# Performance work log

Measured on AMD Instinct MI355X. Metric: run time of the kernel, lower is better.

The kernel has to match this reference:

```python
import jax, jax.numpy as jnp
import numpy as np

EPS = 1e-5

def _instance_norm(x):
    # PyG InstanceNorm with batch=None, affine=False: per-channel normalize
    # over the node/edge dimension with biased variance.
    mean = jnp.mean(x, axis=0, keepdims=True)
    var = jnp.mean(jnp.square(x - mean), axis=0, keepdims=True)
    return (x - mean) * jax.lax.rsqrt(var + EPS)

def setup_inputs() -> dict:
    key = jax.random.key(0)
    ks = jax.random.split(key, 8)
    N, E, H = 50000, 800000, 64
    s1 = 1.0 / np.sqrt(2 * H)
    s2 = 1.0 / np.sqrt(4 * H)
    s3 = 1.0 / np.sqrt(H)
    return {
        "emb": jax.random.normal(ks[0], (N, H), dtype=jnp.float32),
        "edge_index": jax.random.randint(ks[1], (2, E), 0, N, dtype=jnp.int64),
        "W1": jax.random.normal(ks[2], (2 * H, 4 * H), dtype=jnp.float32) * s1,
        "b1": jnp.zeros((4 * H,), dtype=jnp.float32),
        "W2": jax.random.normal(ks[3], (4 * H, H), dtype=jnp.float32) * s2,
        "b2": jnp.zeros((H,), dtype=jnp.float32),
        "W3": jax.random.normal(ks[4], (H, 1), dtype=jnp.float32) * s3,
        "b3": jnp.zeros((1,), dtype=jnp.float32),
    }

def reference(emb, edge_index, W1, b1, W2, b2, W3, b3):
    # Dropout is identity in eval mode.
    col, row = edge_index[0], edge_index[1]
    f12 = jnp.concatenate([emb[col], emb[row]], axis=-1)  # [E, 2H]
    h = jax.nn.relu(_instance_norm(f12 @ W1 + b1))        # [E, 4H]
    h = jax.nn.relu(_instance_norm(h @ W2 + b2))          # [E, H]
    return h @ W3 + b3                                    # [E, 1]
```

## Files before the change

kernel.cpp:

```cpp
#include <hip/hip_runtime.h>
#include <stdint.h>

#define EPS 1e-5f

typedef __attribute__((ext_vector_type(8))) short bf16x8;
typedef __attribute__((ext_vector_type(4))) float f32x4;

__device__ __forceinline__ short f2bf(float f) {
  union { float f; unsigned u; } c; c.f = f;
  unsigned r = (c.u + 0x7FFFu + ((c.u >> 16) & 1u)) >> 16;
  return (short)r;
}
__device__ __forceinline__ float bf2f(unsigned short s) {
  union { unsigned u; float f; } c; c.u = ((unsigned)s) << 16;
  return c.f;
}

#define ASYNC_COPY16(gsrc, ldst)                                                   \
  __builtin_amdgcn_global_load_lds(                                                \
      (const __attribute__((address_space(1))) void*)(gsrc),                       \
      (__attribute__((address_space(3))) void*)(ldst), 16, 0, 0)

#define WS_SUM1 0
#define WS_SQ1  256
#define WS_SUM2 512
#define WS_SQ2  576
#define WS_M1   640
#define WS_I1   896
#define WS_M2   1152
#define WS_I2   1216
#define H2S_BYTE_OFF 8192

__global__ void k_zero(float* ws) {
  for (int i = threadIdx.x; i < 640; i += 256) ws[i] = 0.f;
}

__global__ void k_finalize(float* ws, int n, int so, int qo, int mo, int io, float invE) {
  int j = threadIdx.x;
  if (j < n) {
    float m = ws[so + j] * invE;
    float var = ws[qo + j] * invE - m * m;
    ws[mo + j] = m;
    ws[io + j] = rsqrtf(var + EPS);
  }
}

__global__ __launch_bounds__(256, 2) void k_pass_a(
    const float* __restrict__ emb, const int* __restrict__ ei,
    const float* __restrict__ W1, const float* __restrict__ b1,
    float* __restrict__ ws, char* __restrict__ h1img, int E) {
  extern __shared__ __align__(16) char lds[];
  const int tid = threadIdx.x;
  const int lane = tid & 63;
  const int w = tid >> 6;
  const int l15 = lane & 15;
  const int l4 = lane >> 4;

  bf16x8 B1[4][4];
#pragma unroll
  for (int ni = 0; ni < 4; ++ni)
#pragma unroll
    for (int kk = 0; kk < 4; ++kk) {
      const int c = w * 64 + ni * 16 + l15;
      const int kb = kk * 32 + l4 * 8;
      bf16x8 v;
#pragma unroll
      for (int i = 0; i < 8; ++i) v[i] = f2bf(W1[(kb + i) * 256 + c]);
      B1[ni][kk] = v;
    }
  float b1v[4];
#pragma unroll
  for (int ni = 0; ni < 4; ++ni) b1v[ni] = b1[w * 64 + ni * 16 + l15];

  float sAcc[4] = {0, 0, 0, 0}, qAcc[4] = {0, 0, 0, 0};

  const int nTiles = E >> 6;
  const int e_ = tid >> 2, q_ = tid & 3;

  float4 pf[8];
  {
    const int e0 = blockIdx.x << 6;
    const int nidx = (q_ < 2) ? ei[e0 + e_] : ei[E + e0 + e_];
    const float* src = emb + (long)nidx * 64 + (q_ & 1) * 32;
#pragma unroll
    for (int jj = 0; jj < 8; ++jj)
      pf[jj] = *reinterpret_cast<const float4*>(src + jj * 4);
  }

  for (int t = blockIdx.x; t < nTiles; t += gridDim.x) {
#pragma unroll
    for (int jj = 0; jj < 4; ++jj) {
      bf16x8 p;
      p[0] = f2bf(pf[2 * jj].x); p[1] = f2bf(pf[2 * jj].y);
      p[2] = f2bf(pf[2 * jj].z); p[3] = f2bf(pf[2 * jj].w);
      p[4] = f2bf(pf[2 * jj + 1].x); p[5] = f2bf(pf[2 * jj + 1].y);
      p[6] = f2bf(pf[2 * jj + 1].z); p[7] = f2bf(pf[2 * jj + 1].w);
      int byte = e_ * 256 + q_ * 64 + jj * 16;
      byte ^= (e_ & 7) << 4;
      *reinterpret_cast<bf16x8*>(lds + byte) = p;
    }
    __syncthreads();

    {
      const int tn = t + (int)gridDim.x;
      const int tv = (tn < nTiles) ? tn : t;
      const int e0n = tv << 6;
      const int nidx = (q_ < 2) ? ei[e0n + e_] : ei[E + e0n + e_];
      const float* src = emb + (long)nidx * 64 + (q_ & 1) * 32;
#pragma unroll
      for (int jj = 0; jj < 8; ++jj)
        pf[jj] = *reinterpret_cast<const float4*>(src + jj * 4);
    }

    f32x4 acc[4][4];
#pragma unroll
    for (int mi = 0; mi < 4; ++mi)
#pragma unroll
      for (int ni = 0; ni < 4; ++ni) acc[mi][ni] = f32x4{0.f, 0.f, 0.f, 0.f};
#pragma unroll
    for (int kk = 0; kk < 4; ++kk) {
      bf16x8 af[4];
#pragma unroll
      for (int mi = 0; mi < 4; ++mi) {
        const int row = mi * 16 + l15;
        int byte = row * 256 + kk * 64 + l4 * 16;
        byte ^= (row & 7) << 4;
        af[mi] = *reinterpret_cast<const bf16x8*>(lds + byte);
      }
#pragma unroll
      for (int ni = 0; ni < 4; ++ni)
#pragma unroll
        for (int mi = 0; mi < 4; ++mi)
          acc[mi][ni] = __builtin_amdgcn_mfma_f32_16x16x32_bf16(af[mi], B1[ni][kk], acc[mi][ni], 0, 0, 0);
    }

    char* g = lds + 16384;
#pragma unroll
    for (int mi = 0; mi < 4; ++mi)
#pragma unroll
      for (int ni = 0; ni < 4; ++ni) {
        const int c = w * 64 + ni * 16 + l15;
#pragma unroll
        for (int r = 0; r < 4; ++r) {
          const int row = mi * 16 + l4 * 4 + r;
          const short vb = f2bf(acc[mi][ni][r] + b1v[ni]);
          const float vr = bf2f((unsigned short)vb);
          sAcc[ni] += vr;
          qAcc[ni] += vr * vr;
          int byte = row * 512 + c * 2;
          byte ^= (row & 7) << 4;
          *reinterpret_cast<short*>(g + byte) = vb;
        }
      }
    __syncthreads();

    {
      const char* srcL = lds + 16384 + w * 8192;
      char* dstG = h1img + (size_t)t * 32768 + w * 8192;
#pragma unroll
      for (int r = 0; r < 8; ++r) {
        const bf16x8 v = *reinterpret_cast<const bf16x8*>(srcL + r * 1024 + lane * 16);
        __builtin_nontemporal_store(v, reinterpret_cast<bf16x8*>(dstG + r * 1024 + lane * 16));
      }
    }
  }

#pragma unroll
  for (int ni = 0; ni < 4; ++ni) {
    float s = sAcc[ni], q = qAcc[ni];
    s += __shfl_xor(s, 16); s += __shfl_xor(s, 32);
    q += __shfl_xor(q, 16); q += __shfl_xor(q, 32);
    if (lane < 16) {
      atomicAdd(&ws[WS_SUM1 + w * 64 + ni * 16 + lane], s);
      atomicAdd(&ws[WS_SQ1 + w * 64 + ni * 16 + lane], q);
    }
  }
}

__global__ __launch_bounds__(256, 4) void k_pass_b(
    const char* __restrict__ h1img, const float* __restrict__ W2,
    const float* __restrict__ b2, float* __restrict__ ws,
    unsigned short* __restrict__ h2s, int E) {
  extern __shared__ __align__(16) char lds[];
  const int tid = threadIdx.x;
  const int lane = tid & 63;
  const int w = tid >> 6;
  const int l15 = lane & 15;
  const int l4 = lane >> 4;

  bf16x8 B2[8];
#pragma unroll
  for (int kk = 0; kk < 8; ++kk) {
    const int c = w * 16 + l15;
    const int kb = kk * 32 + l4 * 8;
    bf16x8 v;
#pragma unroll
    for (int i = 0; i < 8; ++i) v[i] = f2bf(W2[(kb + i) * 64 + c]);
    B2[kk] = v;
  }
  const float b2v = b2[w * 16 + l15];

  reinterpret_cast<float*>(lds + 32768)[tid] = ws[WS_M1 + tid];
  reinterpret_cast<float*>(lds + 33792)[tid] = ws[WS_I1 + tid];

  float s2A = 0.f, q2A = 0.f;
  const int nTiles = E >> 6;

  for (int t = blockIdx.x; t < nTiles; t += gridDim.x) {
    __syncthreads();

    {
      const char* src = h1img + (size_t)t * 32768 + w * 8192 + lane * 16;
      char* dst = lds + w * 8192;
#pragma unroll
      for (int r = 0; r < 8; ++r)
        ASYNC_COPY16(src + r * 1024, dst + r * 1024);
    }
    __syncthreads();

    f32x4 acc2[4];
#pragma unroll
    for (int mi = 0; mi < 4; ++mi) acc2[mi] = f32x4{0.f, 0.f, 0.f, 0.f};
#pragma unroll
    for (int kk = 0; kk < 8; ++kk) {
      const int cb = (kk * 32 + l4 * 8) * 4;
      const float4 m1a = *reinterpret_cast<const float4*>(lds + 32768 + cb);
      const float4 m1b = *reinterpret_cast<const float4*>(lds + 32768 + cb + 16);
      const float4 i1a = *reinterpret_cast<const float4*>(lds + 33792 + cb);
      const float4 i1b = *reinterpret_cast<const float4*>(lds + 33792 + cb + 16);
      const float mv[8] = {m1a.x, m1a.y, m1a.z, m1a.w, m1b.x, m1b.y, m1b.z, m1b.w};
      const float iv[8] = {i1a.x, i1a.y, i1a.z, i1a.w, i1b.x, i1b.y, i1b.z, i1b.w};
#pragma unroll
      for (int mi = 0; mi < 4; ++mi) {
        const int row = mi * 16 + l15;
        int byte = row * 512 + kk * 64 + l4 * 16;
        byte ^= (row & 7) << 4;
        const bf16x8 a = *reinterpret_cast<const bf16x8*>(lds + byte);
        bf16x8 an;
#pragma unroll
        for (int i = 0; i < 8; ++i) {
          float v = bf2f((unsigned short)a[i]);
          v = (v - mv[i]) * iv[i];
          an[i] = f2bf(v > 0.f ? v : 0.f);
        }
        acc2[mi] = __builtin_amdgcn_mfma_f32_16x16x32_bf16(an, B2[kk], acc2[mi], 0, 0, 0);
      }
    }
    __syncthreads();

#pragma unroll
    for (int mi = 0; mi < 4; ++mi)
#pragma unroll
      for (int r = 0; r < 4; ++r) {
        const int row = mi * 16 + l4 * 4 + r;
        const float v = acc2[mi][r] + b2v;
        s2A += v;
        q2A += v * v;
        int byte = row * 128 + (w * 16 + l15) * 2;
        byte ^= ((row >> 2) & 3) << 5;
        *reinterpret_cast<short*>(lds + byte) = f2bf(v);
      }
    __syncthreads();

    {
      const int row = tid >> 2, ch = tid & 3;
      const int rb = row * 128 + ((ch * 32) ^ (((row >> 2) & 3) << 5));
      const bf16x8 v0 = *reinterpret_cast<const bf16x8*>(lds + rb);
      const bf16x8 v1 = *reinterpret_cast<const bf16x8*>(lds + rb + 16);
      char* dstG = (char*)h2s + (size_t)t * 8192 + row * 128 + ch * 32;
      __builtin_nontemporal_store(v0, reinterpret_cast<bf16x8*>(dstG));
      __builtin_nontemporal_store(v1, reinterpret_cast<bf16x8*>(dstG + 16));
    }
  }

  {
    float s = s2A, q = q2A;
    s += __shfl_xor(s, 16); s += __shfl_xor(s, 32);
    q += __shfl_xor(q, 16); q += __shfl_xor(q, 32);
    if (lane < 16) {
      atomicAdd(&ws[WS_SUM2 + w * 16 + lane], s);
      atomicAdd(&ws[WS_SQ2 + w * 16 + lane], q);
    }
  }
}

template <int MODE>
__global__ __launch_bounds__(256, 2) void fused_pass(
    const float* __restrict__ emb, const int* __restrict__ ei,
    const float* __restrict__ W1, const float* __restrict__ b1,
    const float* __restrict__ W2, const float* __restrict__ b2,
    const float* __restrict__ W3, const float* __restrict__ b3,
    float* __restrict__ ws, unsigned short* __restrict__ h2s,
    float* __restrict__ out, int E, int storeH2) {
  extern __shared__ __align__(16) char lds[];
  const int tid = threadIdx.x;
  const int lane = tid & 63;
  const int w = tid >> 6;
  const int l15 = lane & 15;
  const int l4 = lane >> 4;

  bf16x8 B1[4][4];
#pragma unroll
  for (int ni = 0; ni < 4; ++ni)
#pragma unroll
    for (int kk = 0; kk < 4; ++kk) {
      const int c = w * 64 + ni * 16 + l15;
      const int kb = kk * 32 + l4 * 8;
      bf16x8 v;
#pragma unroll
      for (int i = 0; i < 8; ++i) v[i] = f2bf(W1[(kb + i) * 256 + c]);
      B1[ni][kk] = v;
    }
  float b1v[4], m1v[4] = {0, 0, 0, 0}, i1v[4] = {0, 0, 0, 0};
#pragma unroll
  for (int ni = 0; ni < 4; ++ni) {
    const int c = w * 64 + ni * 16 + l15;
    b1v[ni] = b1[c];
    if (MODE >= 1) { m1v[ni] = ws[WS_M1 + c]; i1v[ni] = ws[WS_I1 + c]; }
  }
  bf16x8 B2[8];
  float b2v = 0.f, m2v = 0.f, i2v = 0.f, w3v = 0.f;
  if (MODE >= 1) {
#pragma unroll
    for (int kk = 0; kk < 8; ++kk) {
      const int c = w * 16 + l15;
      const int kb = kk * 32 + l4 * 8;
      bf16x8 v;
#pragma unroll
      for (int i = 0; i < 8; ++i) v[i] = f2bf(W2[(kb + i) * 64 + c]);
      B2[kk] = v;
    }
    b2v = b2[w * 16 + l15];
    if (MODE == 2) {
      m2v = ws[WS_M2 + w * 16 + l15];
      i2v = ws[WS_I2 + w * 16 + l15];
      w3v = W3[w * 16 + l15];
    }
  }

  float sAcc[4] = {0, 0, 0, 0}, qAcc[4] = {0, 0, 0, 0};
  float s2A = 0.f, q2A = 0.f;

  const int nTiles = E >> 6;
  for (int t = blockIdx.x; t < nTiles; t += gridDim.x) {
    const int e0 = t << 6;
    __syncthreads();

    {
      const int e = tid >> 2, q = tid & 3;
      const int nidx = (q < 2) ? ei[e0 + e] : ei[E + e0 + e];
      const float* src = emb + (long)nidx * 64 + (q & 1) * 32;
#pragma unroll
      for (int jj = 0; jj < 4; ++jj) {
        float4 fa = *reinterpret_cast<const float4*>(src + jj * 8);
        float4 fb = *reinterpret_cast<const float4*>(src + jj * 8 + 4);
        bf16x8 p;
        p[0] = f2bf(fa.x); p[1] = f2bf(fa.y); p[2] = f2bf(fa.z); p[3] = f2bf(fa.w);
        p[4] = f2bf(fb.x); p[5] = f2bf(fb.y); p[6] = f2bf(fb.z); p[7] = f2bf(fb.w);
        int byte = e * 256 + q * 64 + jj * 16;
        byte ^= (e & 7) << 4;
        *reinterpret_cast<bf16x8*>(lds + byte) = p;
      }
      if (MODE == 2) {
        if (tid < 64) reinterpret_cast<float*>(lds + 49152)[tid] = 0.f;
      }
    }
    __syncthreads();

    f32x4 acc[4][4];
#pragma unroll
    for (int mi = 0; mi < 4; ++mi)
#pragma unroll
      for (int ni = 0; ni < 4; ++ni) acc[mi][ni] = f32x4{0.f, 0.f, 0.f, 0.f};
#pragma unroll
    for (int kk = 0; kk < 4; ++kk) {
      bf16x8 af[4];
#pragma unroll
      for (int mi = 0; mi < 4; ++mi) {
        const int row = mi * 16 + l15;
        int byte = row * 256 + kk * 64 + l4 * 16;
        byte ^= (row & 7) << 4;
        af[mi] = *reinterpret_cast<const bf16x8*>(lds + byte);
      }
#pragma unroll
      for (int ni = 0; ni < 4; ++ni)
#pragma unroll
        for (int mi = 0; mi < 4; ++mi)
          acc[mi][ni] = __builtin_amdgcn_mfma_f32_16x16x32_bf16(af[mi], B1[ni][kk], acc[mi][ni], 0, 0, 0);
    }

    if (MODE == 0) {
#pragma unroll
      for (int mi = 0; mi < 4; ++mi)
#pragma unroll
        for (int ni = 0; ni < 4; ++ni)
#pragma unroll
          for (int r = 0; r < 4; ++r) {
            const float v = acc[mi][ni][r] + b1v[ni];
            sAcc[ni] += v;
            qAcc[ni] += v * v;
          }
    } else {
      char* g = lds + 16384;
#pragma unroll
      for (int mi = 0; mi < 4; ++mi)
#pragma unroll
        for (int ni = 0; ni < 4; ++ni) {
          const int c = w * 64 + ni * 16 + l15;
#pragma unroll
          for (int r = 0; r < 4; ++r) {
            const int row = mi * 16 + l4 * 4 + r;
            float v = (acc[mi][ni][r] + b1v[ni] - m1v[ni]) * i1v[ni];
            v = v > 0.f ? v : 0.f;
            int byte = row * 512 + c * 2;
            byte ^= (row & 7) << 4;
            *reinterpret_cast<short*>(g + byte) = f2bf(v);
          }
        }
      __syncthreads();

      f32x4 acc2[4];
#pragma unroll
      for (int mi = 0; mi < 4; ++mi) acc2[mi] = f32x4{0.f, 0.f, 0.f, 0.f};
#pragma unroll
      for (int kk = 0; kk < 8; ++kk) {
#pragma unroll
        for (int mi = 0; mi < 4; ++mi) {
          const int row = mi * 16 + l15;
          int byte = row * 512 + kk * 64 + l4 * 16;
          byte ^= (row & 7) << 4;
          const bf16x8 a2 = *reinterpret_cast<const bf16x8*>(g + byte);
          acc2[mi] = __builtin_amdgcn_mfma_f32_16x16x32_bf16(a2, B2[kk], acc2[mi], 0, 0, 0);
        }
      }

      if (MODE == 1) {
#pragma unroll
        for (int mi = 0; mi < 4; ++mi)
#pragma unroll
          for (int r = 0; r < 4; ++r) {
            const float v = acc2[mi][r] + b2v;
            s2A += v;
            q2A += v * v;
            if (storeH2) {
              const int row = e0 + mi * 16 + l4 * 4 + r;
              h2s[(size_t)row * 64 + w * 16 + l15] = (unsigned short)f2bf(v);
            }
          }
      } else {
        float* outp = reinterpret_cast<float*>(lds + 49152);
#pragma unroll
        for (int mi = 0; mi < 4; ++mi)
#pragma unroll
          for (int r = 0; r < 4; ++r) {
            const float v = acc2[mi][r] + b2v;
            float z = (v - m2v) * i2v;
            z = z > 0.f ? z : 0.f;
            float pv = z * w3v;
            pv += __shfl_xor(pv, 1);
            pv += __shfl_xor(pv, 2);
            pv += __shfl_xor(pv, 4);
            pv += __shfl_xor(pv, 8);
            if (l15 == 0) atomicAdd(&outp[mi * 16 + l4 * 4 + r], pv);
          }
        __syncthreads();
        if (tid < 64) out[e0 + tid] = outp[tid] + b3[0];
      }
    }
  }

  if (MODE == 0) {
#pragma unroll
    for (int ni = 0; ni < 4; ++ni) {
      float s = sAcc[ni], q = qAcc[ni];
      s += __shfl_xor(s, 16); s += __shfl_xor(s, 32);
      q += __shfl_xor(q, 16); q += __shfl_xor(q, 32);
      if (lane < 16) {
        atomicAdd(&ws[WS_SUM1 + w * 64 + ni * 16 + lane], s);
        atomicAdd(&ws[WS_SQ1 + w * 64 + ni * 16 + lane], q);
      }
    }
  }
  if (MODE == 1) {
    float s = s2A, q = q2A;
    s += __shfl_xor(s, 16); s += __shfl_xor(s, 32);
    q += __shfl_xor(q, 16); q += __shfl_xor(q, 32);
    if (lane < 16) {
      atomicAdd(&ws[WS_SUM2 + w * 16 + lane], s);
      atomicAdd(&ws[WS_SQ2 + w * 16 + lane], q);
    }
  }
}

__global__ void k_out(const unsigned short* __restrict__ h2s, const float* __restrict__ ws,
                      const float* __restrict__ W3, const float* __restrict__ b3,
                      float* __restrict__ out, int E) {
  __shared__ float sm[64], si[64], sw[64];
  const int tid = threadIdx.x;
  if (tid < 64) {
    sm[tid] = ws[WS_M2 + tid];
    si[tid] = ws[WS_I2 + tid];
    sw[tid] = W3[tid];
  }
  __syncthreads();
  const int e = blockIdx.x * 256 + tid;
  if (e >= E) return;
  const unsigned short* rp = h2s + (size_t)e * 64;
  float a = 0.f;
#pragma unroll
  for (int jj = 0; jj < 8; ++jj) {
    const bf16x8 v8 = *reinterpret_cast<const bf16x8*>(rp + jj * 8);
#pragma unroll
    for (int i = 0; i < 8; ++i) {
      const int j = jj * 8 + i;
      const float v = bf2f((unsigned short)v8[i]);
      float z = (v - sm[j]) * si[j];
      z = z > 0.f ? z : 0.f;
      a += z * sw[j];
    }
  }
  out[e] = a + b3[0];
}

extern "C" void kernel_launch(void* const* d_in, const int* in_sizes, int n_in,
                              void* d_out, int out_size, void* d_ws, size_t ws_size,
                              hipStream_t stream) {
  (void)n_in; (void)out_size;
  const float* emb = (const float*)d_in[0];
  const int* ei = (const int*)d_in[1];
  const float* W1 = (const float*)d_in[2];
  const float* b1 = (const float*)d_in[3];
  const float* W2 = (const float*)d_in[4];
  const float* b2 = (const float*)d_in[5];
  const float* W3 = (const float*)d_in[6];
  const float* b3 = (const float*)d_in[7];
  float* out = (float*)d_out;
  float* ws = (float*)d_ws;
  unsigned short* h2s = (unsigned short*)((char*)d_ws + H2S_BYTE_OFF);

  const int E = in_sizes[1] / 2;
  const size_t h2bytes = (size_t)E * 64 * 2;
  const size_t h1bytes = (size_t)E * 256 * 2;
  char* h1img = (char*)d_ws + H2S_BYTE_OFF + h2bytes;
  const int storeH2 = (ws_size >= (size_t)H2S_BYTE_OFF + h2bytes) ? 1 : 0;
  const int storeH1 = (ws_size >= (size_t)H2S_BYTE_OFF + h2bytes + h1bytes) ? 1 : 0;
  const float invE = 1.0f / (float)E;

  k_zero<<<1, 256, 0, stream>>>(ws);
  if (storeH1) {
    k_pass_a<<<1024, 256, 49152, stream>>>(emb, ei, W1, b1, ws, h1img, E);
    k_finalize<<<1, 256, 0, stream>>>(ws, 256, WS_SUM1, WS_SQ1, WS_M1, WS_I1, invE);
    k_pass_b<<<2048, 256, 34816, stream>>>(h1img, W2, b2, ws, h2s, E);
    k_finalize<<<1, 256, 0, stream>>>(ws, 64, WS_SUM2, WS_SQ2, WS_M2, WS_I2, invE);
    k_out<<<(E + 255) / 256, 256, 0, stream>>>(h2s, ws, W3, b3, out, E);
  } else {
    fused_pass<0><<<768, 256, 16384, stream>>>(emb, ei, W1, b1, W2, b2, W3, b3, ws, h2s, out, E, storeH2);
    k_finalize<<<1, 256, 0, stream>>>(ws, 256, WS_SUM1, WS_SQ1, WS_M1, WS_I1, invE);
    fused_pass<1><<<512, 256, 49152, stream>>>(emb, ei, W1, b1, W2, b2, W3, b3, ws, h2s, out, E, storeH2);
    k_finalize<<<1, 256, 0, stream>>>(ws, 64, WS_SUM2, WS_SQ2, WS_M2, WS_I2, invE);
    if (storeH2)
      k_out<<<(E + 255) / 256, 256, 0, stream>>>(h2s, ws, W3, b3, out, E);
    else
      fused_pass<2><<<512, 256, 49408, stream>>>(emb, ei, W1, b1, W2, b2, W3, b3, ws, h2s, out, E, storeH2);
  }
}
```

Before: 844.0 us.

## Store gathered bf16 inputs instead of layer-1 activations and recompute GEMM1 in pass B

Pass A now writes the gathered, concatenated bf16 edge features (128 channels) to workspace instead of the 256-channel layer-1 pre-activation, which halves that intermediate's write and read traffic. Pass B reloads these features with double-buffered async LDS copies, recomputes the first GEMM with W1 held in registers, applies normalization and ReLU in registers, and feeds the second GEMM. The cost is doing the first matmul twice and holding extra registers, so occupancy drops to 2 blocks with 64KB of LDS. Statistics for layer 1 are now taken on fp32 values rather than bf16-rounded ones.

```diff
diff --git a/kernel.cpp b/kernel.cpp
--- a/kernel.cpp
+++ b/kernel.cpp
@@ -48,7 +48,7 @@
 __global__ __launch_bounds__(256, 2) void k_pass_a(
     const float* __restrict__ emb, const int* __restrict__ ei,
     const float* __restrict__ W1, const float* __restrict__ b1,
-    float* __restrict__ ws, char* __restrict__ h1img, int E) {
+    float* __restrict__ ws, char* __restrict__ f12img, int E) {
   extern __shared__ __align__(16) char lds[];
   const int tid = threadIdx.x;
   const int lane = tid & 63;
@@ -112,6 +112,16 @@
         pf[jj] = *reinterpret_cast<const float4*>(src + jj * 4);
     }
 
+    {
+      const char* srcL = lds + w * 4096 + lane * 16;
+      char* dstG = f12img + (size_t)t * 16384 + w * 4096 + lane * 16;
+#pragma unroll
+      for (int r = 0; r < 4; ++r) {
+        const bf16x8 v = *reinterpret_cast<const bf16x8*>(srcL + r * 1024);
+        __builtin_nontemporal_store(v, reinterpret_cast<bf16x8*>(dstG + r * 1024));
+      }
+    }
+
     f32x4 acc[4][4];
 #pragma unroll
     for (int mi = 0; mi < 4; ++mi)
@@ -134,35 +144,17 @@
           acc[mi][ni] = __builtin_amdgcn_mfma_f32_16x16x32_bf16(af[mi], B1[ni][kk], acc[mi][ni], 0, 0, 0);
     }
 
-    char* g = lds + 16384;
 #pragma unroll
     for (int mi = 0; mi < 4; ++mi)
 #pragma unroll
-      for (int ni = 0; ni < 4; ++ni) {
-        const int c = w * 64 + ni * 16 + l15;
+      for (int ni = 0; ni < 4; ++ni)
 #pragma unroll
         for (int r = 0; r < 4; ++r) {
-          const int row = mi * 16 + l4 * 4 + r;
-          const short vb = f2bf(acc[mi][ni][r] + b1v[ni]);
-          const float vr = bf2f((unsigned short)vb);
-          sAcc[ni] += vr;
-          qAcc[ni] += vr * vr;
-          int byte = row * 512 + c * 2;
-          byte ^= (row & 7) << 4;
-          *reinterpret_cast<short*>(g + byte) = vb;
+          const float v = acc[mi][ni][r] + b1v[ni];
+          sAcc[ni] += v;
+          qAcc[ni] += v * v;
         }
-      }
     __syncthreads();
-
-    {
-      const char* srcL = lds + 16384 + w * 8192;
-      char* dstG = h1img + (size_t)t * 32768 + w * 8192;
-#pragma unroll
-      for (int r = 0; r < 8; ++r) {
-        const bf16x8 v = *reinterpret_cast<const bf16x8*>(srcL + r * 1024 + lane * 16);
-        __builtin_nontemporal_store(v, reinterpret_cast<bf16x8*>(dstG + r * 1024 + lane * 16));
-      }
-    }
   }
 
 #pragma unroll
@@ -177,10 +169,11 @@
   }
 }
 
-__global__ __launch_bounds__(256, 4) void k_pass_b(
-    const char* __restrict__ h1img, const float* __restrict__ W2,
-    const float* __restrict__ b2, float* __restrict__ ws,
-    unsigned short* __restrict__ h2s, int E) {
+__global__ __launch_bounds__(256, 2) void k_pass_b(
+    const char* __restrict__ f12img,
+    const float* __restrict__ W1, const float* __restrict__ b1,
+    const float* __restrict__ W2, const float* __restrict__ b2,
+    float* __restrict__ ws, unsigned short* __restrict__ h2s, int E) {
   extern __shared__ __align__(16) char lds[];
   const int tid = threadIdx.x;
   const int lane = tid & 63;
@@ -188,6 +181,26 @@
   const int l15 = lane & 15;
   const int l4 = lane >> 4;
 
+  bf16x8 B1[4][4];
+#pragma unroll
+  for (int ni = 0; ni < 4; ++ni)
+#pragma unroll
+    for (int kk = 0; kk < 4; ++kk) {
+      const int c = w * 64 + ni * 16 + l15;
+      const int kb = kk * 32 + l4 * 8;
+      bf16x8 v;
+#pragma unroll
+      for (int i = 0; i < 8; ++i) v[i] = f2bf(W1[(kb + i) * 256 + c]);
+      B1[ni][kk] = v;
+    }
+  float b1v[4], m1v[4], i1v[4];
+#pragma unroll
+  for (int ni = 0; ni < 4; ++ni) {
+    const int c = w * 64 + ni * 16 + l15;
+    b1v[ni] = b1[c];
+    m1v[ni] = ws[WS_M1 + c];
+    i1v[ni] = ws[WS_I1 + c];
+  }
   bf16x8 B2[8];
 #pragma unroll
   for (int kk = 0; kk < 8; ++kk) {
@@ -200,22 +213,69 @@
   }
   const float b2v = b2[w * 16 + l15];
 
-  reinterpret_cast<float*>(lds + 32768)[tid] = ws[WS_M1 + tid];
-  reinterpret_cast<float*>(lds + 33792)[tid] = ws[WS_I1 + tid];
-
   float s2A = 0.f, q2A = 0.f;
   const int nTiles = E >> 6;
 
+  {
+    const char* src = f12img + (size_t)blockIdx.x * 16384 + w * 4096 + lane * 16;
+    char* dst = lds + w * 4096 + lane * 16;
+#pragma unroll
+    for (int r = 0; r < 4; ++r) ASYNC_COPY16(src + r * 1024, dst + r * 1024);
+  }
+
+  int cur = 0;
   for (int t = blockIdx.x; t < nTiles; t += gridDim.x) {
     __syncthreads();
 
     {
-      const char* src = h1img + (size_t)t * 32768 + w * 8192 + lane * 16;
-      char* dst = lds + w * 8192;
-#pragma unroll
-      for (int r = 0; r < 8; ++r)
-        ASYNC_COPY16(src + r * 1024, dst + r * 1024);
-    }
+      const int tn = t + (int)gridDim.x;
+      if (tn < nTiles) {
+        const char* src = f12img + (size_t)tn * 16384 + w * 4096 + lane * 16;
+        char* dst = lds + (cur ^ 1) * 16384 + w * 4096 + lane * 16;
+#pragma unroll
+        for (int r = 0; r < 4; ++r) ASYNC_COPY16(src + r * 1024, dst + r * 1024);
+      }
+    }
+
+    const char* Ab = lds + cur * 16384;
+    f32x4 acc[4][4];
+#pragma unroll
+    for (int mi = 0; mi < 4; ++mi)
+#pragma unroll
+      for (int ni = 0; ni < 4; ++ni) acc[mi][ni] = f32x4{0.f, 0.f, 0.f, 0.f};
+#pragma unroll
+    for (int kk = 0; kk < 4; ++kk) {
+      bf16x8 af[4];
+#pragma unroll
+      for (int mi = 0; mi < 4; ++mi) {
+        const int row = mi * 16 + l15;
+        int byte = row * 256 + kk * 64 + l4 * 16;
+        byte ^= (row & 7) << 4;
+        af[mi] = *reinterpret_cast<const bf16x8*>(Ab + byte);
+      }
+#pragma unroll
+      for (int ni = 0; ni < 4; ++ni)
+#pragma unroll
+        for (int mi = 0; mi < 4; ++mi)
+          acc[mi][ni] = __builtin_amdgcn_mfma_f32_16x16x32_bf16(af[mi], B1[ni][kk], acc[mi][ni], 0, 0, 0);
+    }
+
+    char* g = lds + 32768;
+#pragma unroll
+    for (int mi = 0; mi < 4; ++mi)
+#pragma unroll
+      for (int ni = 0; ni < 4; ++ni) {
+        const int c = w * 64 + ni * 16 + l15;
+#pragma unroll
+        for (int r = 0; r < 4; ++r) {
+          const int row = mi * 16 + l4 * 4 + r;
+          float v = (acc[mi][ni][r] + b1v[ni] - m1v[ni]) * i1v[ni];
+          v = v > 0.f ? v : 0.f;
+          int byte = row * 512 + c * 2;
+          byte ^= (row & 7) << 4;
+          *reinterpret_cast<short*>(g + byte) = f2bf(v);
+        }
+      }
     __syncthreads();
 
     f32x4 acc2[4];
@@ -223,31 +283,17 @@
     for (int mi = 0; mi < 4; ++mi) acc2[mi] = f32x4{0.f, 0.f, 0.f, 0.f};
 #pragma unroll
     for (int kk = 0; kk < 8; ++kk) {
-      const int cb = (kk * 32 + l4 * 8) * 4;
-      const float4 m1a = *reinterpret_cast<const float4*>(lds + 32768 + cb);
-      const float4 m1b = *reinterpret_cast<const float4*>(lds + 32768 + cb + 16);
-      const float4 i1a = *reinterpret_cast<const float4*>(lds + 33792 + cb);
-      const float4 i1b = *reinterpret_cast<const float4*>(lds + 33792 + cb + 16);
-      const float mv[8] = {m1a.x, m1a.y, m1a.z, m1a.w, m1b.x, m1b.y, m1b.z, m1b.w};
-      const float iv[8] = {i1a.x, i1a.y, i1a.z, i1a.w, i1b.x, i1b.y, i1b.z, i1b.w};
 #pragma unroll
       for (int mi = 0; mi < 4; ++mi) {
         const int row = mi * 16 + l15;
         int byte = row * 512 + kk * 64 + l4 * 16;
         byte ^= (row & 7) << 4;
-        const bf16x8 a = *reinterpret_cast<const bf16x8*>(lds + byte);
-        bf16x8 an;
-#pragma unroll
-        for (int i = 0; i < 8; ++i) {
-          float v = bf2f((unsigned short)a[i]);
-          v = (v - mv[i]) * iv[i];
-          an[i] = f2bf(v > 0.f ? v : 0.f);
-        }
-        acc2[mi] = __builtin_amdgcn_mfma_f32_16x16x32_bf16(an, B2[kk], acc2[mi], 0, 0, 0);
-      }
-    }
-    __syncthreads();
-
+        const bf16x8 a2 = *reinterpret_cast<const bf16x8*>(g + byte);
+        acc2[mi] = __builtin_amdgcn_mfma_f32_16x16x32_bf16(a2, B2[kk], acc2[mi], 0, 0, 0);
+      }
+    }
+
+    char* bb = lds + cur * 16384;
 #pragma unroll
     for (int mi = 0; mi < 4; ++mi)
 #pragma unroll
@@ -258,19 +304,20 @@
         q2A += v * v;
         int byte = row * 128 + (w * 16 + l15) * 2;
         byte ^= ((row >> 2) & 3) << 5;
-        *reinterpret_cast<short*>(lds + byte) = f2bf(v);
+        *reinterpret_cast<short*>(bb + byte) = f2bf(v);
       }
     __syncthreads();
 
     {
       const int row = tid >> 2, ch = tid & 3;
-      const int rb = row * 128 + ((ch * 32) ^ (((row >> 2) & 3) << 5));
+      const int rb = cur * 16384 + row * 128 + ((ch * 32) ^ (((row >> 2) & 3) << 5));
       const bf16x8 v0 = *reinterpret_cast<const bf16x8*>(lds + rb);
       const bf16x8 v1 = *reinterpret_cast<const bf16x8*>(lds + rb + 16);
       char* dstG = (char*)h2s + (size_t)t * 8192 + row * 128 + ch * 32;
       __builtin_nontemporal_store(v0, reinterpret_cast<bf16x8*>(dstG));
       __builtin_nontemporal_store(v1, reinterpret_cast<bf16x8*>(dstG + 16));
     }
+    cur ^= 1;
   }
 
   {
@@ -540,17 +587,17 @@
 
   const int E = in_sizes[1] / 2;
   const size_t h2bytes = (size_t)E * 64 * 2;
-  const size_t h1bytes = (size_t)E * 256 * 2;
-  char* h1img = (char*)d_ws + H2S_BYTE_OFF + h2bytes;
+  const size_t f12bytes = (size_t)E * 128 * 2;
+  char* f12img = (char*)d_ws + H2S_BYTE_OFF + h2bytes;
   const int storeH2 = (ws_size >= (size_t)H2S_BYTE_OFF + h2bytes) ? 1 : 0;
-  const int storeH1 = (ws_size >= (size_t)H2S_BYTE_OFF + h2bytes + h1bytes) ? 1 : 0;
+  const int storeF12 = (ws_size >= (size_t)H2S_BYTE_OFF + h2bytes + f12bytes) ? 1 : 0;
   const float invE = 1.0f / (float)E;
 
   k_zero<<<1, 256, 0, stream>>>(ws);
-  if (storeH1) {
-    k_pass_a<<<1024, 256, 49152, stream>>>(emb, ei, W1, b1, ws, h1img, E);
+  if (storeF12) {
+    k_pass_a<<<1024, 256, 16384, stream>>>(emb, ei, W1, b1, ws, f12img, E);
     k_finalize<<<1, 256, 0, stream>>>(ws, 256, WS_SUM1, WS_SQ1, WS_M1, WS_I1, invE);
-    k_pass_b<<<2048, 256, 34816, stream>>>(h1img, W2, b2, ws, h2s, E);
+    k_pass_b<<<1024, 256, 65536, stream>>>(f12img, W1, b1, W2, b2, ws, h2s, E);
     k_finalize<<<1, 256, 0, stream>>>(ws, 64, WS_SUM2, WS_SQ2, WS_M2, WS_I2, invE);
     k_out<<<(E + 255) / 256, 256, 0, stream>>>(h2s, ws, W3, b3, out, E);
   } else {
```

Result: no change. 845.6 us (+0.2%).
